# Performance work log

Measured on AMD Instinct MI355X. Metric: run time of the kernel, lower is better.

Reference implementation:

```python
import jax, jax.numpy as jnp
import numpy as np
import math

H = 256  # hidden dim hardcoded in module; d_k = 256
EPS = 1e-5  # torch LayerNorm eps


def _mlp2(x, W1, b1, W2, b2):
    # nn.Sequential(Linear, Tanh, Linear, Tanh)
    return jnp.tanh(jnp.tanh(x @ W1 + b1) @ W2 + b2)


def _ln(x, w, b):
    mu = x.mean(-1, keepdims=True)
    var = ((x - mu) ** 2).mean(-1, keepdims=True)
    return (x - mu) / jnp.sqrt(var + EPS) * w + b


def setup_inputs():
    B, N, D, A = 128, 32, 128, 16
    key = jax.random.key(0)
    ks = jax.random.split(key, 32)

    def lin(k, i, o):
        return jax.random.normal(k, (i, o), jnp.float32) / np.sqrt(i).astype(np.float32)

    inp = {
        'states': jax.random.normal(ks[0], (B, N, D), jnp.float32),
        'policies': jax.nn.softmax(jax.random.normal(ks[1], (B, N, A), jnp.float32), axis=-1),
        'actions': jax.nn.one_hot(jax.random.randint(ks[2], (B, N), 0, A), A, dtype=jnp.float32),
    }
    # two-layer MLP params: state_embed(se), key(k), query(q), state_act_embed(sa),
    # attention_value(av), curr_agent_state_embed(ca)
    ins = {'se': D, 'k': H, 'q': H, 'sa': D + A, 'av': H, 'ca': D}
    i = 3
    for n in ['se', 'k', 'q', 'sa', 'av', 'ca']:
        inp[n + '_W1'] = lin(ks[i], ins[n], H); inp[n + '_b1'] = jnp.zeros((H,), jnp.float32)
        inp[n + '_W2'] = lin(ks[i + 1], H, H);  inp[n + '_b2'] = jnp.zeros((H,), jnp.float32)
        i += 2
    inp['f_W1'] = lin(ks[i], 2 * H, H); inp['f_b1'] = jnp.zeros((H,), jnp.float32); i += 1
    inp['f_W2'] = lin(ks[i], H, H);     inp['f_b2'] = jnp.zeros((H,), jnp.float32); i += 1
    inp['f_W3'] = lin(ks[i], H, A);     inp['f_b3'] = jnp.zeros((A,), jnp.float32); i += 1
    inp['ln1_w'] = jnp.ones((H,), jnp.float32); inp['ln1_b'] = jnp.zeros((H,), jnp.float32)
    inp['ln2_w'] = jnp.ones((H,), jnp.float32); inp['ln2_b'] = jnp.zeros((H,), jnp.float32)
    return inp


def reference(states, policies, actions,
              se_W1, se_b1, se_W2, se_b2,
              k_W1, k_b1, k_W2, k_b2,
              q_W1, q_b1, q_W2, q_b2,
              sa_W1, sa_b1, sa_W2, sa_b2,
              av_W1, av_b1, av_W2, av_b2,
              ca_W1, ca_b1, ca_W2, ca_b2,
              f_W1, f_b1, f_W2, f_b2, f_W3, f_b3,
              ln1_w, ln1_b, ln2_w, ln2_b):
    B, N, D = states.shape
    # remove_self_loops: per-agent gather of all other agents (static index map)
    nbr = np.array([[j for j in range(N) if j != i] for i in range(N)])  # [N, N-1]
    states_key = states[:, nbr, :]        # [B,N,N-1,D]
    actions_nb = actions[:, nbr, :]       # [B,N,N-1,A]
    obs_actions = jnp.concatenate([states_key, actions_nb], axis=-1)

    sq_embed = _mlp2(states, se_W1, se_b1, se_W2, se_b2)       # [B,N,256] (query path)
    sk_embed = _mlp2(states_key, se_W1, se_b1, se_W2, se_b2)   # [B,N,N-1,256]
    key_obs = _mlp2(sk_embed, k_W1, k_b1, k_W2, k_b2)          # [B,N,N-1,256]
    query_obs = _mlp2(sq_embed, q_W1, q_b1, q_W2, q_b2)        # [B,N,256]

    scores = jnp.einsum('bnd,bnmd->bnm', query_obs, key_obs) / math.sqrt(float(H))
    weight = jax.nn.softmax(scores, axis=-1)                   # [B,N,N-1]

    # weight_assignment: insert 1.0 at the self position
    rows = np.arange(N)[:, None]
    weights_full = jnp.zeros((B, N, N), weight.dtype).at[:, rows, nbr].set(weight)
    weights_full = weights_full.at[:, np.arange(N), np.arange(N)].set(1.0)

    oa_embed = _mlp2(obs_actions, sa_W1, sa_b1, sa_W2, sa_b2)  # [B,N,N-1,256]
    att_vals = _mlp2(oa_embed, av_W1, av_b1, av_W2, av_b2)     # [B,N,N-1,256]
    node_feat = jnp.einsum('bnm,bnmd->bnd', weight, att_vals)  # [B,N,256]
    node_feat = _ln(oa_embed.mean(axis=-2) + node_feat, ln1_w, ln1_b)

    cur = _mlp2(states, ca_W1, ca_b1, ca_W2, ca_b2)
    cur = _ln(cur + sk_embed.mean(axis=-2) + sq_embed, ln2_w, ln2_b)

    feat = jnp.concatenate([cur, node_feat], axis=-1)          # [B,N,512]
    h = jnp.tanh(feat @ f_W1 + f_b1)
    h = jnp.tanh(h @ f_W2 + f_b2)
    Q = h @ f_W3 + f_b3                                        # [B,N,A]

    Value = jnp.einsum('bna,bma->bnm', Q, policies)            # Q @ policies^T -> [B,N,N]
    Q_value = jnp.sum(actions * Q, axis=-1, keepdims=True)     # [B,N,1]
    return Value, Q_value, weights_full
```

## Files before the change

kernel.cpp:

```cpp
#include <hip/hip_runtime.h>
#include <hip/hip_bf16.h>


struct Ptrs37 { const void* p[37]; };
struct Meta37 { int sz[37]; unsigned off[37]; };
struct PrepW  { int widx[14]; unsigned dstOff[14]; int K[14]; int Kp[14]; };

typedef __attribute__((ext_vector_type(8))) short bf16x8;
typedef __attribute__((ext_vector_type(4))) float f32x4;

__device__ __forceinline__ bool is_bf16_env(const void* ln1w) {
  return (*(const unsigned int*)ln1w) != 0x3f800000u;
}
__device__ __forceinline__ unsigned short f2bf(float f) {
  union { __hip_bfloat16 h; unsigned short u; } cv;
  cv.h = __float2bfloat16(f);
  return cv.u;
}
__device__ __forceinline__ float bf2f(unsigned short s) {
  return __uint_as_float(((unsigned int)s) << 16);
}
__device__ __forceinline__ float4 ldbf4(const unsigned short* p) {
  uint2 u = *(const uint2*)p;
  const unsigned short* s = (const unsigned short*)&u;
  return make_float4(bf2f(s[0]), bf2f(s[1]), bf2f(s[2]), bf2f(s[3]));
}

__global__ __launch_bounds__(256) void prep_all_kernel(Ptrs37 P, Meta37 M, PrepW pw,
                                                       float* __restrict__ F,
                                                       unsigned short* __restrict__ WT,
                                                       unsigned short* __restrict__ OAin) {
  bool bf = is_bf16_env(P.p[33]);
  int y = blockIdx.y;
  int stride = gridDim.x * 256;
  int g0 = blockIdx.x * 256 + threadIdx.x;
  if (y < 37) {
    int n = M.sz[y];
    float* dst = F + M.off[y];
    if (bf) {
      const unsigned short* s = (const unsigned short*)P.p[y];
      for (int idx = g0; idx < n; idx += stride)
        dst[idx] = __uint_as_float(((unsigned int)s[idx]) << 16);
    } else {
      const float* s = (const float*)P.p[y];
      for (int idx = g0; idx < n; idx += stride) dst[idx] = s[idx];
    }
  } else if (y < 51) {
    int t = y - 37;
    const void* src = P.p[pw.widx[t]];
    unsigned short* dst = WT + pw.dstOff[t];
    int K = pw.K[t], Kp = pw.Kp[t];
    int total = 256 * Kp;
    for (int idx = g0; idx < total; idx += stride) {
      int n = idx / Kp, k = idx - n * Kp;
      unsigned short v = 0;
      if (k < K) {
        size_t si = (size_t)k * 256 + n;
        v = bf ? ((const unsigned short*)src)[si] : f2bf(((const float*)src)[si]);
      }
      dst[idx] = v;
    }
  } else {
    const void* S = P.p[0];
    const void* A = P.p[2];
    for (int gid = g0; gid < 4096 * 160; gid += stride) {
      int r = gid / 160, c = gid - r * 160;
      unsigned short v = 0;
      if (c < 128) {
        size_t si = (size_t)r * 128 + c;
        v = bf ? ((const unsigned short*)S)[si] : f2bf(((const float*)S)[si]);
      } else if (c < 144) {
        size_t si = (size_t)r * 16 + (c - 128);
        v = bf ? ((const unsigned short*)A)[si] : f2bf(((const float*)A)[si]);
      }
      OAin[gid] = v;
    }
  }
}

struct GemmDesc {
  const unsigned short* X; const unsigned short* WT; const float* bias;
  unsigned short* Y; int K; int ldx;
};
struct GemmStage { GemmDesc g[3]; };

__global__ __launch_bounds__(256) void gemm_mfma_kernel(GemmStage st) {
  GemmDesc d = st.g[blockIdx.z];
  const unsigned short* __restrict__ X = d.X;
  const unsigned short* __restrict__ WT = d.WT;
  const int K = d.K;
  __shared__ uint4 AsB[2][256];
  __shared__ uint4 BsB[2][256];
  const int tid = threadIdx.x;
  const int l = tid & 63, w = tid >> 6;
  const int m0 = blockIdx.y << 6, n0 = blockIdx.x << 6;
  const int wm = w >> 1, wn = w & 1;
  const int arow = wm * 32 + (l & 15);
  const int brow = wn * 32 + (l & 15);
  const int koff = (l >> 4) * 8;
  const unsigned short* ag = X + (size_t)(m0 + (tid >> 2)) * d.ldx + (tid & 3) * 8;
  const unsigned short* bg = WT + (size_t)(n0 + (tid >> 2)) * K + (tid & 3) * 8;
  f32x4 acc[2][2] = {};
  AsB[0][tid] = *(const uint4*)ag;
  BsB[0][tid] = *(const uint4*)bg;
  __syncthreads();
  int cur = 0;
  for (int k0 = 0; k0 < K; k0 += 32) {
    const bool more = (k0 + 32) < K;
    uint4 na, nb;
    if (more) {
      na = *(const uint4*)(ag + k0 + 32);
      nb = *(const uint4*)(bg + k0 + 32);
    }
    const char* Ab = (const char*)AsB[cur];
    const char* Bb = (const char*)BsB[cur];
    bf16x8 a0 = *(const bf16x8*)(Ab + arow * 64 + koff * 2);
    bf16x8 a1 = *(const bf16x8*)(Ab + (arow + 16) * 64 + koff * 2);
    bf16x8 b0 = *(const bf16x8*)(Bb + brow * 64 + koff * 2);
    bf16x8 b1 = *(const bf16x8*)(Bb + (brow + 16) * 64 + koff * 2);
    acc[0][0] = __builtin_amdgcn_mfma_f32_16x16x32_bf16(a0, b0, acc[0][0], 0, 0, 0);
    acc[0][1] = __builtin_amdgcn_mfma_f32_16x16x32_bf16(a0, b1, acc[0][1], 0, 0, 0);
    acc[1][0] = __builtin_amdgcn_mfma_f32_16x16x32_bf16(a1, b0, acc[1][0], 0, 0, 0);
    acc[1][1] = __builtin_amdgcn_mfma_f32_16x16x32_bf16(a1, b1, acc[1][1], 0, 0, 0);
    if (more) {
      AsB[cur ^ 1][tid] = na;
      BsB[cur ^ 1][tid] = nb;
      __syncthreads();
      cur ^= 1;
    }
  }
  const float* __restrict__ Bv = d.bias;
  __hip_bfloat16* __restrict__ Y = (__hip_bfloat16*)d.Y;
  const int col0 = n0 + wn * 32 + (l & 15);
  const int rbase = m0 + wm * 32 + (l >> 4) * 4;
#pragma unroll
  for (int ni = 0; ni < 2; ++ni) {
    int col = col0 + ni * 16;
    float bias = Bv[col];
#pragma unroll
    for (int mi = 0; mi < 2; ++mi) {
#pragma unroll
      for (int r = 0; r < 4; ++r) {
        int row = rbase + mi * 16 + r;
        Y[(size_t)row * 256 + col] = __float2bfloat16(tanhf(acc[mi][ni][r] + bias));
      }
    }
  }
}

__global__ __launch_bounds__(256) void attn_kernel(
    const unsigned short* __restrict__ Qb, const unsigned short* __restrict__ Kb,
    const unsigned short* __restrict__ AVp, const unsigned short* __restrict__ OAp,
    const unsigned short* __restrict__ SEp,
    float* __restrict__ NF, float* __restrict__ sumOA, float* __restrict__ sumSE,
    void* __restrict__ dout, const void* __restrict__ ln1w) {
  const size_t WF_OFF = 135168;
  int b = blockIdx.x;
  int tid = threadIdx.x;
  bool bf = is_bf16_env(ln1w);
  __shared__ float AVs[32 * 260];
  __shared__ float wsT[32][36];

  const unsigned short* avg = AVp + (size_t)b * 8192;
  for (int i = tid * 4; i < 8192; i += 1024) {
    int j = i >> 8, c = i & 255;
    *(float4*)&AVs[j * 260 + c] = ldbf4(avg + i);
  }
  {
    int c = tid;
    float sa = 0.f, ss = 0.f;
    const unsigned short* oab = OAp + (size_t)b * 8192 + c;
    const unsigned short* seb = SEp + (size_t)b * 8192 + c;
#pragma unroll 4
    for (int j = 0; j < 32; ++j) { sa += bf2f(oab[j * 256]); ss += bf2f(seb[j * 256]); }
    sumOA[b * 256 + c] = sa;
    sumSE[b * 256 + c] = ss;
  }

  int l = tid & 63, w = tid >> 6;
  int j = l & 31, h = l >> 5;
  const unsigned short* kbase = Kb + (size_t)b * 8192 + j * 256 + h * 128;
  const unsigned short* qbase = Qb + (size_t)b * 8192 + h * 128;
  for (int q = 0; q < 2; ++q) {
    int n0 = w * 8 + q * 4;
    float acc0 = 0.f, acc1 = 0.f, acc2 = 0.f, acc3 = 0.f;
    for (int t = 0; t < 32; ++t) {
      float4 kv = ldbf4(kbase + t * 4);
      float4 q0 = ldbf4(qbase + (n0 + 0) * 256 + t * 4);
      float4 q1 = ldbf4(qbase + (n0 + 1) * 256 + t * 4);
      float4 q2 = ldbf4(qbase + (n0 + 2) * 256 + t * 4);
      float4 q3 = ldbf4(qbase + (n0 + 3) * 256 + t * 4);
      acc0 += q0.x * kv.x + q0.y * kv.y + q0.z * kv.z + q0.w * kv.w;
      acc1 += q1.x * kv.x + q1.y * kv.y + q1.z * kv.z + q1.w * kv.w;
      acc2 += q2.x * kv.x + q2.y * kv.y + q2.z * kv.z + q2.w * kv.w;
      acc3 += q3.x * kv.x + q3.y * kv.y + q3.z * kv.z + q3.w * kv.w;
    }
#pragma unroll
    for (int i = 0; i < 4; ++i) {
      float part = (i == 0) ? acc0 : (i == 1) ? acc1 : (i == 2) ? acc2 : acc3;
      float full = part + __shfl_down(part, 32);
      int n = n0 + i;
      float sc = full * 0.0625f;
      if (j == n) sc = -1e30f;
      float mx = sc;
      mx = fmaxf(mx, __shfl_xor(mx, 16));
      mx = fmaxf(mx, __shfl_xor(mx, 8));
      mx = fmaxf(mx, __shfl_xor(mx, 4));
      mx = fmaxf(mx, __shfl_xor(mx, 2));
      mx = fmaxf(mx, __shfl_xor(mx, 1));
      float e = __expf(sc - mx);
      float s = e;
      s += __shfl_xor(s, 16); s += __shfl_xor(s, 8); s += __shfl_xor(s, 4);
      s += __shfl_xor(s, 2);  s += __shfl_xor(s, 1);
      float wgt = e / s;
      if (l < 32) {
        wsT[j][n] = wgt;
        size_t oi = WF_OFF + ((size_t)(b * 32 + n)) * 32 + j;
        float ov = (j == n) ? 1.0f : wgt;
        if (bf) ((__hip_bfloat16*)dout)[oi] = __float2bfloat16(ov);
        else    ((float*)dout)[oi] = ov;
      }
    }
  }
  __syncthreads();

  int tx = tid & 63, tyy = tid >> 6;
  float accn[8][4] = {};
  for (int jj = 0; jj < 32; ++jj) {
    float4 av = *(const float4*)&AVs[jj * 260 + (tx << 2)];
    const float* wr = &wsT[jj][tyy * 8];
#pragma unroll
    for (int g = 0; g < 8; ++g) {
      float wv = wr[g];
      accn[g][0] += av.x * wv; accn[g][1] += av.y * wv;
      accn[g][2] += av.z * wv; accn[g][3] += av.w * wv;
    }
  }
#pragma unroll
  for (int g = 0; g < 8; ++g) {
    float4 o = make_float4(accn[g][0], accn[g][1], accn[g][2], accn[g][3]);
    *(float4*)&NF[((size_t)(b * 32 + tyy * 8 + g)) * 256 + (tx << 2)] = o;
  }
}

__global__ __launch_bounds__(64) void ln_kernel(
    const float* __restrict__ NF, const float* __restrict__ sOA, const unsigned short* __restrict__ OAp,
    const unsigned short* __restrict__ Cc, const float* __restrict__ sSE, const unsigned short* __restrict__ SEp,
    const float* __restrict__ w1, const float* __restrict__ b1,
    const float* __restrict__ w2, const float* __restrict__ b2,
    unsigned short* __restrict__ feat) {
  int row = blockIdx.x, b = row >> 5, l = threadIdx.x;
  float x[4], y[4];
#pragma unroll
  for (int i = 0; i < 4; ++i) {
    int c = l + (i << 6);
    float oa = bf2f(OAp[row * 256 + c]);
    float se = bf2f(SEp[row * 256 + c]);
    x[i] = NF[row * 256 + c] + (sOA[b * 256 + c] - oa) * (1.0f / 31.0f);
    y[i] = bf2f(Cc[row * 256 + c]) + (sSE[b * 256 + c] - se) * (1.0f / 31.0f) + se;
  }
  float sx = x[0] + x[1] + x[2] + x[3];
  float sy = y[0] + y[1] + y[2] + y[3];
  for (int d = 1; d < 64; d <<= 1) { sx += __shfl_xor(sx, d); sy += __shfl_xor(sy, d); }
  float mx = sx * (1.0f / 256.0f), my = sy * (1.0f / 256.0f);
  float vx = 0.f, vy = 0.f;
#pragma unroll
  for (int i = 0; i < 4; ++i) {
    float dx = x[i] - mx; vx += dx * dx;
    float dy = y[i] - my; vy += dy * dy;
  }
  for (int d = 1; d < 64; d <<= 1) { vx += __shfl_xor(vx, d); vy += __shfl_xor(vy, d); }
  float rx = rsqrtf(vx * (1.0f / 256.0f) + 1e-5f);
  float ry = rsqrtf(vy * (1.0f / 256.0f) + 1e-5f);
#pragma unroll
  for (int i = 0; i < 4; ++i) {
    int c = l + (i << 6);
    feat[(size_t)row * 512 + 256 + c] = f2bf((x[i] - mx) * rx * w1[c] + b1[c]);
    feat[(size_t)row * 512 + c]       = f2bf((y[i] - my) * ry * w2[c] + b2[c]);
  }
}

__global__ __launch_bounds__(256) void qfinal_kernel(const unsigned short* __restrict__ H2,
                                                     const float* __restrict__ W3,
                                                     const float* __restrict__ b3,
                                                     const float* __restrict__ POL,
                                                     const float* __restrict__ ACT,
                                                     void* __restrict__ dout,
                                                     const void* __restrict__ ln1w) {
  bool bf = is_bf16_env(ln1w);
  int b = blockIdx.x, tid = threadIdx.x;
  __shared__ float h2s[32 * 256];
  __shared__ float w3s[256 * 16];
  __shared__ float qfs[512], pols[512], acts[512];
  {
    const unsigned short* src = H2 + (size_t)b * 8192;
#pragma unroll
    for (int i = 0; i < 4; ++i) {
      int base = (tid + i * 256) * 8;
      uint4 u = *(const uint4*)(src + base);
      const unsigned short* s = (const unsigned short*)&u;
#pragma unroll
      for (int e = 0; e < 8; ++e) h2s[base + e] = bf2f(s[e]);
    }
    const float4* wsrc = (const float4*)W3;
    float4* wdst = (float4*)w3s;
#pragma unroll
    for (int i = 0; i < 4; ++i) wdst[tid + i * 256] = wsrc[tid + i * 256];
  }
  for (int i = tid; i < 512; i += 256) {
    pols[i] = POL[(size_t)b * 512 + i];
    acts[i] = ACT[(size_t)b * 512 + i];
  }
  __syncthreads();
#pragma unroll
  for (int t = 0; t < 2; ++t) {
    int p = tid + t * 256;
    int row = p >> 4, a = p & 15;
    float acc = b3[a];
#pragma unroll 8
    for (int k = 0; k < 256; ++k) acc += h2s[row * 256 + k] * w3s[k * 16 + a];
    qfs[p] = acc;
  }
  __syncthreads();
#pragma unroll
  for (int r = 0; r < 4; ++r) {
    int p = tid + (r << 8);
    int n = p >> 5, m = p & 31;
    float acc = 0.f;
#pragma unroll
    for (int a = 0; a < 16; ++a) acc += qfs[n * 16 + a] * pols[m * 16 + a];
    size_t oi = (size_t)b * 1024 + p;
    if (bf) ((__hip_bfloat16*)dout)[oi] = __float2bfloat16(acc);
    else    ((float*)dout)[oi] = acc;
  }
  if (tid < 32) {
    float acc = 0.f;
#pragma unroll
    for (int a = 0; a < 16; ++a) acc += acts[tid * 16 + a] * qfs[tid * 16 + a];
    size_t oi = 131072 + (size_t)b * 32 + tid;
    if (bf) ((__hip_bfloat16*)dout)[oi] = __float2bfloat16(acc);
    else    ((float*)dout)[oi] = acc;
  }
}

extern "C" void kernel_launch(void* const* d_in, const int* in_sizes, int n_in,
                              void* d_out, int out_size, void* d_ws, size_t ws_size,
                              hipStream_t stream) {
  (void)n_in; (void)out_size; (void)ws_size;
  Ptrs37 P; Meta37 M;
  unsigned off = 0;
  for (int i = 0; i < 37; ++i) {
    P.p[i] = d_in[i];
    M.sz[i] = in_sizes[i];
    M.off[i] = off;
    off += (unsigned)in_sizes[i];
  }
  float* F = (float*)d_ws;
  const unsigned MEG = 1048576u;
  unsigned X0 = (off + 511u) & ~511u;
  auto BUF = [&](int slot) { return (unsigned short*)(F + X0 + slot * MEG); };
  unsigned short* SE   = BUF(0);
  unsigned short* QB   = BUF(1);
  unsigned short* KB   = BUF(2);
  unsigned short* OA   = BUF(3);
  unsigned short* AV   = BUF(4);
  unsigned short* CC   = BUF(5);
  unsigned short* T1   = BUF(6);
  unsigned short* T2   = BUF(7);
  unsigned short* T3   = BUF(8);
  float*          NF   = F + X0 + 9 * MEG;
  unsigned short* FEAT = BUF(10);
  unsigned short* OAIN = BUF(12);
  unsigned short* H1   = BUF(13);
  unsigned short* H2   = BUF(14);
  float* SOA  = F + X0 + 15 * MEG;
  float* SSE  = SOA + 32768;
  unsigned short* WT = (unsigned short*)(F + X0 + 16 * MEG);
  auto Wp = [&](int i) { return F + M.off[i]; };
  const void* ln1w_raw = d_in[33];

  static const int wIdx[14] = {3,5,7,9,11,13,15,17,19,21,23,25,27,29};
  PrepW pw{};
  unsigned wtOff[37] = {};
  int Kp_[37] = {};
  unsigned cum = 0;
  for (int t = 0; t < 14; ++t) {
    int i = wIdx[t];
    int K = in_sizes[i] / 256;
    int Kp = (K + 31) & ~31;
    pw.widx[t] = i;
    pw.dstOff[t] = cum;
    pw.K[t] = K; pw.Kp[t] = Kp;
    wtOff[i] = cum; Kp_[i] = Kp;
    cum += (unsigned)(256 * Kp);
  }

  prep_all_kernel<<<dim3(64, 52), 256, 0, stream>>>(P, M, pw, F, WT, OAIN);

  auto G = [&](const unsigned short* X, int ldx, int wi, int bi, unsigned short* Y) {
    GemmDesc g; g.X = X; g.WT = WT + wtOff[wi]; g.bias = Wp(bi); g.Y = Y;
    g.K = Kp_[wi]; g.ldx = ldx;
    return g;
  };
  dim3 gg3(4, 64, 3), gg1(4, 64, 1);
  GemmStage s1{{ G(OAIN, 160, 3, 4, T1),  G(OAIN, 160, 15, 16, T2), G(OAIN, 160, 23, 24, T3) }};
  gemm_mfma_kernel<<<gg3, 256, 0, stream>>>(s1);
  GemmStage s2{{ G(T1, 256, 5, 6, SE),  G(T2, 256, 17, 18, OA),  G(T3, 256, 25, 26, CC) }};
  gemm_mfma_kernel<<<gg3, 256, 0, stream>>>(s2);
  GemmStage s3{{ G(SE, 256, 7, 8, T1),  G(SE, 256, 11, 12, T2),  G(OA, 256, 19, 20, T3) }};
  gemm_mfma_kernel<<<gg3, 256, 0, stream>>>(s3);
  GemmStage s4{{ G(T1, 256, 9, 10, KB), G(T2, 256, 13, 14, QB), G(T3, 256, 21, 22, AV) }};
  gemm_mfma_kernel<<<gg3, 256, 0, stream>>>(s4);

  attn_kernel<<<128, 256, 0, stream>>>(QB, KB, AV, OA, SE, NF, SOA, SSE, d_out, ln1w_raw);
  ln_kernel<<<4096, 64, 0, stream>>>(NF, SOA, OA, CC, SSE, SE,
                                     Wp(33), Wp(34), Wp(35), Wp(36), FEAT);

  GemmDesc g5 = G(FEAT, 512, 27, 28, H1);
  GemmStage s5{{ g5, g5, g5 }};
  gemm_mfma_kernel<<<gg1, 256, 0, stream>>>(s5);
  GemmDesc g6 = G(H1, 256, 29, 30, H2);
  GemmStage s6{{ g6, g6, g6 }};
  gemm_mfma_kernel<<<gg1, 256, 0, stream>>>(s6);

  qfinal_kernel<<<128, 256, 0, stream>>>(H2, Wp(31), Wp(32),
                                         F + M.off[1], F + M.off[2], d_out, ln1w_raw);
}
```

Measured before the change: 237.8 us.

## Fuse two-layer MLP GEMM pairs, attention with LayerNorm, and tail MLP into single kernels

Replaces the per-layer GEMM launches with an mlp2 kernel that computes both linear+tanh layers for a 32-row tile, keeping the intermediate activations in shared memory. Attention and LayerNorm are merged so node features and column sums stay in LDS. The final two GEMMs and the Q/Value computation are merged into one tail kernel. This removes several launches and the global round trips for intermediates. In exchange, grids shrink to 384 or 128 blocks, and each block reloads the full weight matrices.

Result: slower. 287.3 us (+20.8%).

```diff
diff --git a/kernel.cpp b/kernel.cpp
--- a/kernel.cpp
+++ b/kernel.cpp
@@ -78,81 +78,148 @@
   }
 }
 
-struct GemmDesc {
-  const unsigned short* X; const unsigned short* WT; const float* bias;
-  unsigned short* Y; int K; int ldx;
+struct Mlp2Desc {
+  const unsigned short* X; int ldx; int K1;
+  const unsigned short* W1T; const float* b1;
+  const unsigned short* W2T; const float* b2;
+  unsigned short* Y;
 };
-struct GemmStage { GemmDesc g[3]; };
-
-__global__ __launch_bounds__(256) void gemm_mfma_kernel(GemmStage st) {
-  GemmDesc d = st.g[blockIdx.z];
-  const unsigned short* __restrict__ X = d.X;
-  const unsigned short* __restrict__ WT = d.WT;
-  const int K = d.K;
-  __shared__ uint4 AsB[2][256];
-  __shared__ uint4 BsB[2][256];
+struct Mlp2Stage { Mlp2Desc g[3]; };
+
+__global__ __launch_bounds__(256) void mlp2_kernel(Mlp2Stage st) {
+  Mlp2Desc d = st.g[blockIdx.y];
   const int tid = threadIdx.x;
   const int l = tid & 63, w = tid >> 6;
-  const int m0 = blockIdx.y << 6, n0 = blockIdx.x << 6;
-  const int wm = w >> 1, wn = w & 1;
-  const int arow = wm * 32 + (l & 15);
-  const int brow = wn * 32 + (l & 15);
-  const int koff = (l >> 4) * 8;
-  const unsigned short* ag = X + (size_t)(m0 + (tid >> 2)) * d.ldx + (tid & 3) * 8;
-  const unsigned short* bg = WT + (size_t)(n0 + (tid >> 2)) * K + (tid & 3) * 8;
-  f32x4 acc[2][2] = {};
-  AsB[0][tid] = *(const uint4*)ag;
-  BsB[0][tid] = *(const uint4*)bg;
-  __syncthreads();
-  int cur = 0;
-  for (int k0 = 0; k0 < K; k0 += 32) {
-    const bool more = (k0 + 32) < K;
-    uint4 na, nb;
-    if (more) {
-      na = *(const uint4*)(ag + k0 + 32);
-      nb = *(const uint4*)(bg + k0 + 32);
-    }
-    const char* Ab = (const char*)AsB[cur];
-    const char* Bb = (const char*)BsB[cur];
-    bf16x8 a0 = *(const bf16x8*)(Ab + arow * 64 + koff * 2);
-    bf16x8 a1 = *(const bf16x8*)(Ab + (arow + 16) * 64 + koff * 2);
-    bf16x8 b0 = *(const bf16x8*)(Bb + brow * 64 + koff * 2);
-    bf16x8 b1 = *(const bf16x8*)(Bb + (brow + 16) * 64 + koff * 2);
-    acc[0][0] = __builtin_amdgcn_mfma_f32_16x16x32_bf16(a0, b0, acc[0][0], 0, 0, 0);
-    acc[0][1] = __builtin_amdgcn_mfma_f32_16x16x32_bf16(a0, b1, acc[0][1], 0, 0, 0);
-    acc[1][0] = __builtin_amdgcn_mfma_f32_16x16x32_bf16(a1, b0, acc[1][0], 0, 0, 0);
-    acc[1][1] = __builtin_amdgcn_mfma_f32_16x16x32_bf16(a1, b1, acc[1][1], 0, 0, 0);
-    if (more) {
-      AsB[cur ^ 1][tid] = na;
-      BsB[cur ^ 1][tid] = nb;
-      __syncthreads();
-      cur ^= 1;
-    }
-  }
-  const float* __restrict__ Bv = d.bias;
-  __hip_bfloat16* __restrict__ Y = (__hip_bfloat16*)d.Y;
-  const int col0 = n0 + wn * 32 + (l & 15);
-  const int rbase = m0 + wm * 32 + (l >> 4) * 4;
-#pragma unroll
-  for (int ni = 0; ni < 2; ++ni) {
-    int col = col0 + ni * 16;
-    float bias = Bv[col];
-#pragma unroll
-    for (int mi = 0; mi < 2; ++mi) {
-#pragma unroll
-      for (int r = 0; r < 4; ++r) {
-        int row = rbase + mi * 16 + r;
-        Y[(size_t)row * 256 + col] = __float2bfloat16(tanhf(acc[mi][ni][r] + bias));
-      }
-    }
-  }
-}
-
-__global__ __launch_bounds__(256) void attn_kernel(
+  const int lane16 = l & 15, quad = l >> 4;
+  const int m0 = blockIdx.x << 5;
+  __shared__ uint4 A1[2][128];
+  __shared__ uint4 Bt[2][1024];
+  __shared__ unsigned short Y1[32 * 264];
+  const int bcol = tid >> 2, bchk = tid & 3;
+  {
+    const int K1 = d.K1;
+    const unsigned short* ag = d.X + (size_t)(m0 + (tid >> 2)) * d.ldx + (tid & 3) * 8;
+    const unsigned short* w1 = d.W1T;
+    f32x4 acc[2][4] = {};
+    if (tid < 128) A1[0][tid] = *(const uint4*)ag;
+#pragma unroll
+    for (int i = 0; i < 4; ++i) {
+      int c = bcol + (i << 6);
+      Bt[0][c * 4 + bchk] = *(const uint4*)(w1 + (size_t)c * K1 + bchk * 8);
+    }
+    __syncthreads();
+    int cur = 0;
+    for (int k0 = 0; k0 < K1; k0 += 32) {
+      const bool more = (k0 + 32) < K1;
+      uint4 na, nb[4];
+      if (more) {
+        if (tid < 128) na = *(const uint4*)(ag + k0 + 32);
+#pragma unroll
+        for (int i = 0; i < 4; ++i) {
+          int c = bcol + (i << 6);
+          nb[i] = *(const uint4*)(w1 + (size_t)c * K1 + k0 + 32 + bchk * 8);
+        }
+      }
+      const char* Ab = (const char*)A1[cur];
+      const char* Bb = (const char*)Bt[cur];
+      bf16x8 a0 = *(const bf16x8*)(Ab + lane16 * 64 + quad * 16);
+      bf16x8 a1 = *(const bf16x8*)(Ab + (lane16 + 16) * 64 + quad * 16);
+#pragma unroll
+      for (int ni = 0; ni < 4; ++ni) {
+        int cc = (w << 6) + ni * 16 + lane16;
+        bf16x8 b = *(const bf16x8*)(Bb + cc * 64 + quad * 16);
+        acc[0][ni] = __builtin_amdgcn_mfma_f32_16x16x32_bf16(a0, b, acc[0][ni], 0, 0, 0);
+        acc[1][ni] = __builtin_amdgcn_mfma_f32_16x16x32_bf16(a1, b, acc[1][ni], 0, 0, 0);
+      }
+      if (more) {
+        if (tid < 128) A1[cur ^ 1][tid] = na;
+#pragma unroll
+        for (int i = 0; i < 4; ++i) {
+          int c = bcol + (i << 6);
+          Bt[cur ^ 1][c * 4 + bchk] = nb[i];
+        }
+        __syncthreads();
+        cur ^= 1;
+      }
+    }
+#pragma unroll
+    for (int ni = 0; ni < 4; ++ni) {
+      int col = (w << 6) + ni * 16 + lane16;
+      float bias = d.b1[col];
+#pragma unroll
+      for (int mi = 0; mi < 2; ++mi) {
+#pragma unroll
+        for (int r = 0; r < 4; ++r) {
+          int row = mi * 16 + quad * 4 + r;
+          Y1[row * 264 + col] = f2bf(tanhf(acc[mi][ni][r] + bias));
+        }
+      }
+    }
+  }
+  __syncthreads();
+  {
+    const unsigned short* w2 = d.W2T;
+    f32x4 acc[2][4] = {};
+#pragma unroll
+    for (int i = 0; i < 4; ++i) {
+      int c = bcol + (i << 6);
+      Bt[0][c * 4 + bchk] = *(const uint4*)(w2 + (size_t)c * 256 + bchk * 8);
+    }
+    __syncthreads();
+    int cur = 0;
+    for (int k0 = 0; k0 < 256; k0 += 32) {
+      const bool more = (k0 + 32) < 256;
+      uint4 nb[4];
+      if (more) {
+#pragma unroll
+        for (int i = 0; i < 4; ++i) {
+          int c = bcol + (i << 6);
+          nb[i] = *(const uint4*)(w2 + (size_t)c * 256 + k0 + 32 + bchk * 8);
+        }
+      }
+      const char* Bb = (const char*)Bt[cur];
+      bf16x8 a0 = *(const bf16x8*)(Y1 + lane16 * 264 + k0 + quad * 8);
+      bf16x8 a1 = *(const bf16x8*)(Y1 + (lane16 + 16) * 264 + k0 + quad * 8);
+#pragma unroll
+      for (int ni = 0; ni < 4; ++ni) {
+        int cc = (w << 6) + ni * 16 + lane16;
+        bf16x8 b = *(const bf16x8*)(Bb + cc * 64 + quad * 16);
+        acc[0][ni] = __builtin_amdgcn_mfma_f32_16x16x32_bf16(a0, b, acc[0][ni], 0, 0, 0);
+        acc[1][ni] = __builtin_amdgcn_mfma_f32_16x16x32_bf16(a1, b, acc[1][ni], 0, 0, 0);
+      }
+      if (more) {
+#pragma unroll
+        for (int i = 0; i < 4; ++i) {
+          int c = bcol + (i << 6);
+          Bt[cur ^ 1][c * 4 + bchk] = nb[i];
+        }
+        __syncthreads();
+        cur ^= 1;
+      }
+    }
+#pragma unroll
+    for (int ni = 0; ni < 4; ++ni) {
+      int col = (w << 6) + ni * 16 + lane16;
+      float bias = d.b2[col];
+#pragma unroll
+      for (int mi = 0; mi < 2; ++mi) {
+#pragma unroll
+        for (int r = 0; r < 4; ++r) {
+          int row = m0 + mi * 16 + quad * 4 + r;
+          d.Y[(size_t)row * 256 + col] = f2bf(tanhf(acc[mi][ni][r] + bias));
+        }
+      }
+    }
+  }
+}
+
+__global__ __launch_bounds__(256) void attnln_kernel(
     const unsigned short* __restrict__ Qb, const unsigned short* __restrict__ Kb,
     const unsigned short* __restrict__ AVp, const unsigned short* __restrict__ OAp,
-    const unsigned short* __restrict__ SEp,
-    float* __restrict__ NF, float* __restrict__ sumOA, float* __restrict__ sumSE,
+    const unsigned short* __restrict__ SEp, const unsigned short* __restrict__ Cc,
+    const float* __restrict__ w1, const float* __restrict__ b1,
+    const float* __restrict__ w2, const float* __restrict__ b2,
+    unsigned short* __restrict__ feat,
     void* __restrict__ dout, const void* __restrict__ ln1w) {
   const size_t WF_OFF = 135168;
   int b = blockIdx.x;
@@ -160,6 +227,7 @@
   bool bf = is_bf16_env(ln1w);
   __shared__ float AVs[32 * 260];
   __shared__ float wsT[32][36];
+  __shared__ float sOAs[256], sSEs[256];
 
   const unsigned short* avg = AVp + (size_t)b * 8192;
   for (int i = tid * 4; i < 8192; i += 1024) {
@@ -173,8 +241,8 @@
     const unsigned short* seb = SEp + (size_t)b * 8192 + c;
 #pragma unroll 4
     for (int j = 0; j < 32; ++j) { sa += bf2f(oab[j * 256]); ss += bf2f(seb[j * 256]); }
-    sumOA[b * 256 + c] = sa;
-    sumSE[b * 256 + c] = ss;
+    sOAs[c] = sa;
+    sSEs[c] = ss;
   }
 
   int l = tid & 63, w = tid >> 6;
@@ -236,80 +304,180 @@
       accn[g][2] += av.z * wv; accn[g][3] += av.w * wv;
     }
   }
+  __syncthreads();
 #pragma unroll
   for (int g = 0; g < 8; ++g) {
     float4 o = make_float4(accn[g][0], accn[g][1], accn[g][2], accn[g][3]);
-    *(float4*)&NF[((size_t)(b * 32 + tyy * 8 + g)) * 256 + (tx << 2)] = o;
-  }
-}
-
-__global__ __launch_bounds__(64) void ln_kernel(
-    const float* __restrict__ NF, const float* __restrict__ sOA, const unsigned short* __restrict__ OAp,
-    const unsigned short* __restrict__ Cc, const float* __restrict__ sSE, const unsigned short* __restrict__ SEp,
-    const float* __restrict__ w1, const float* __restrict__ b1,
-    const float* __restrict__ w2, const float* __restrict__ b2,
-    unsigned short* __restrict__ feat) {
-  int row = blockIdx.x, b = row >> 5, l = threadIdx.x;
-  float x[4], y[4];
-#pragma unroll
-  for (int i = 0; i < 4; ++i) {
-    int c = l + (i << 6);
-    float oa = bf2f(OAp[row * 256 + c]);
-    float se = bf2f(SEp[row * 256 + c]);
-    x[i] = NF[row * 256 + c] + (sOA[b * 256 + c] - oa) * (1.0f / 31.0f);
-    y[i] = bf2f(Cc[row * 256 + c]) + (sSE[b * 256 + c] - se) * (1.0f / 31.0f) + se;
-  }
-  float sx = x[0] + x[1] + x[2] + x[3];
-  float sy = y[0] + y[1] + y[2] + y[3];
-  for (int d = 1; d < 64; d <<= 1) { sx += __shfl_xor(sx, d); sy += __shfl_xor(sy, d); }
-  float mx = sx * (1.0f / 256.0f), my = sy * (1.0f / 256.0f);
-  float vx = 0.f, vy = 0.f;
-#pragma unroll
-  for (int i = 0; i < 4; ++i) {
-    float dx = x[i] - mx; vx += dx * dx;
-    float dy = y[i] - my; vy += dy * dy;
-  }
-  for (int d = 1; d < 64; d <<= 1) { vx += __shfl_xor(vx, d); vy += __shfl_xor(vy, d); }
-  float rx = rsqrtf(vx * (1.0f / 256.0f) + 1e-5f);
-  float ry = rsqrtf(vy * (1.0f / 256.0f) + 1e-5f);
-#pragma unroll
-  for (int i = 0; i < 4; ++i) {
-    int c = l + (i << 6);
-    feat[(size_t)row * 512 + 256 + c] = f2bf((x[i] - mx) * rx * w1[c] + b1[c]);
-    feat[(size_t)row * 512 + c]       = f2bf((y[i] - my) * ry * w2[c] + b2[c]);
-  }
-}
-
-__global__ __launch_bounds__(256) void qfinal_kernel(const unsigned short* __restrict__ H2,
-                                                     const float* __restrict__ W3,
-                                                     const float* __restrict__ b3,
-                                                     const float* __restrict__ POL,
-                                                     const float* __restrict__ ACT,
-                                                     void* __restrict__ dout,
-                                                     const void* __restrict__ ln1w) {
+    *(float4*)&AVs[(tyy * 8 + g) * 260 + (tx << 2)] = o;
+  }
+  __syncthreads();
+
+  for (int r = w; r < 32; r += 4) {
+    int row = b * 32 + r;
+    float x[4], y[4];
+#pragma unroll
+    for (int i = 0; i < 4; ++i) {
+      int c = l + (i << 6);
+      float oa = bf2f(OAp[(size_t)row * 256 + c]);
+      float se = bf2f(SEp[(size_t)row * 256 + c]);
+      x[i] = AVs[r * 260 + c] + (sOAs[c] - oa) * (1.0f / 31.0f);
+      y[i] = bf2f(Cc[(size_t)row * 256 + c]) + (sSEs[c] - se) * (1.0f / 31.0f) + se;
+    }
+    float sx = x[0] + x[1] + x[2] + x[3];
+    float sy = y[0] + y[1] + y[2] + y[3];
+    for (int dd = 1; dd < 64; dd <<= 1) { sx += __shfl_xor(sx, dd); sy += __shfl_xor(sy, dd); }
+    float mx = sx * (1.0f / 256.0f), my = sy * (1.0f / 256.0f);
+    float vx = 0.f, vy = 0.f;
+#pragma unroll
+    for (int i = 0; i < 4; ++i) {
+      float dx = x[i] - mx; vx += dx * dx;
+      float dy = y[i] - my; vy += dy * dy;
+    }
+    for (int dd = 1; dd < 64; dd <<= 1) { vx += __shfl_xor(vx, dd); vy += __shfl_xor(vy, dd); }
+    float rx = rsqrtf(vx * (1.0f / 256.0f) + 1e-5f);
+    float ry = rsqrtf(vy * (1.0f / 256.0f) + 1e-5f);
+#pragma unroll
+    for (int i = 0; i < 4; ++i) {
+      int c = l + (i << 6);
+      feat[(size_t)row * 512 + 256 + c] = f2bf((x[i] - mx) * rx * w1[c] + b1[c]);
+      feat[(size_t)row * 512 + c]       = f2bf((y[i] - my) * ry * w2[c] + b2[c]);
+    }
+  }
+}
+
+__global__ __launch_bounds__(256) void tail_kernel(
+    const unsigned short* __restrict__ FEAT,
+    const unsigned short* __restrict__ W1T,
+    const float* __restrict__ fb1,
+    const unsigned short* __restrict__ W2T,
+    const float* __restrict__ fb2,
+    const float* __restrict__ W3,
+    const float* __restrict__ b3,
+    const float* __restrict__ POL, const float* __restrict__ ACT,
+    void* __restrict__ dout, const void* __restrict__ ln1w) {
   bool bf = is_bf16_env(ln1w);
   int b = blockIdx.x, tid = threadIdx.x;
-  __shared__ float h2s[32 * 256];
-  __shared__ float w3s[256 * 16];
-  __shared__ float qfs[512], pols[512], acts[512];
-  {
-    const unsigned short* src = H2 + (size_t)b * 8192;
-#pragma unroll
-    for (int i = 0; i < 4; ++i) {
-      int base = (tid + i * 256) * 8;
-      uint4 u = *(const uint4*)(src + base);
-      const unsigned short* s = (const unsigned short*)&u;
-#pragma unroll
-      for (int e = 0; e < 8; ++e) h2s[base + e] = bf2f(s[e]);
-    }
-    const float4* wsrc = (const float4*)W3;
-    float4* wdst = (float4*)w3s;
-#pragma unroll
-    for (int i = 0; i < 4; ++i) wdst[tid + i * 256] = wsrc[tid + i * 256];
-  }
+  const int l = tid & 63, w = tid >> 6;
+  const int lane16 = l & 15, quad = l >> 4;
+  __shared__ uint4 Bt[1024];
+  __shared__ unsigned short H1[32 * 264];
+  __shared__ unsigned short H2[32 * 256];
+  __shared__ float qfs[512];
+  __shared__ float pols[512], acts[512];
+  const int bcol = tid >> 2, bchk = tid & 3;
   for (int i = tid; i < 512; i += 256) {
     pols[i] = POL[(size_t)b * 512 + i];
     acts[i] = ACT[(size_t)b * 512 + i];
+  }
+  {
+    const unsigned short* ax0 = FEAT + (size_t)(b * 32 + lane16) * 512 + quad * 8;
+    const unsigned short* ax1 = ax0 + (size_t)16 * 512;
+    f32x4 acc[2][4] = {};
+    uint4 a0c = *(const uint4*)ax0;
+    uint4 a1c = *(const uint4*)ax1;
+#pragma unroll
+    for (int i = 0; i < 4; ++i) {
+      int c = bcol + (i << 6);
+      Bt[c * 4 + bchk] = *(const uint4*)(W1T + (size_t)c * 512 + bchk * 8);
+    }
+    __syncthreads();
+    for (int k0 = 0; k0 < 512; k0 += 32) {
+      const bool more = (k0 + 32) < 512;
+      uint4 na0, na1, nb[4];
+      if (more) {
+        na0 = *(const uint4*)(ax0 + k0 + 32);
+        na1 = *(const uint4*)(ax1 + k0 + 32);
+#pragma unroll
+        for (int i = 0; i < 4; ++i) {
+          int c = bcol + (i << 6);
+          nb[i] = *(const uint4*)(W1T + (size_t)c * 512 + k0 + 32 + bchk * 8);
+        }
+      }
+      bf16x8 a0 = *(const bf16x8*)&a0c;
+      bf16x8 a1 = *(const bf16x8*)&a1c;
+#pragma unroll
+      for (int ni = 0; ni < 4; ++ni) {
+        int cc = (w << 6) + ni * 16 + lane16;
+        bf16x8 bb = *(const bf16x8*)((const char*)Bt + cc * 64 + quad * 16);
+        acc[0][ni] = __builtin_amdgcn_mfma_f32_16x16x32_bf16(a0, bb, acc[0][ni], 0, 0, 0);
+        acc[1][ni] = __builtin_amdgcn_mfma_f32_16x16x32_bf16(a1, bb, acc[1][ni], 0, 0, 0);
+      }
+      if (more) {
+        __syncthreads();
+#pragma unroll
+        for (int i = 0; i < 4; ++i) {
+          int c = bcol + (i << 6);
+          Bt[c * 4 + bchk] = nb[i];
+        }
+        a0c = na0; a1c = na1;
+        __syncthreads();
+      }
+    }
+#pragma unroll
+    for (int ni = 0; ni < 4; ++ni) {
+      int col = (w << 6) + ni * 16 + lane16;
+      float bias = fb1[col];
+#pragma unroll
+      for (int mi = 0; mi < 2; ++mi) {
+#pragma unroll
+        for (int r = 0; r < 4; ++r) {
+          int row = mi * 16 + quad * 4 + r;
+          H1[row * 264 + col] = f2bf(tanhf(acc[mi][ni][r] + bias));
+        }
+      }
+    }
+  }
+  __syncthreads();
+  {
+    f32x4 acc[2][4] = {};
+#pragma unroll
+    for (int i = 0; i < 4; ++i) {
+      int c = bcol + (i << 6);
+      Bt[c * 4 + bchk] = *(const uint4*)(W2T + (size_t)c * 256 + bchk * 8);
+    }
+    __syncthreads();
+    for (int k0 = 0; k0 < 256; k0 += 32) {
+      const bool more = (k0 + 32) < 256;
+      uint4 nb[4];
+      if (more) {
+#pragma unroll
+        for (int i = 0; i < 4; ++i) {
+          int c = bcol + (i << 6);
+          nb[i] = *(const uint4*)(W2T + (size_t)c * 256 + k0 + 32 + bchk * 8);
+        }
+      }
+      bf16x8 a0 = *(const bf16x8*)(H1 + lane16 * 264 + k0 + quad * 8);
+      bf16x8 a1 = *(const bf16x8*)(H1 + (lane16 + 16) * 264 + k0 + quad * 8);
+#pragma unroll
+      for (int ni = 0; ni < 4; ++ni) {
+        int cc = (w << 6) + ni * 16 + lane16;
+        bf16x8 bb = *(const bf16x8*)((const char*)Bt + cc * 64 + quad * 16);
+        acc[0][ni] = __builtin_amdgcn_mfma_f32_16x16x32_bf16(a0, bb, acc[0][ni], 0, 0, 0);
+        acc[1][ni] = __builtin_amdgcn_mfma_f32_16x16x32_bf16(a1, bb, acc[1][ni], 0, 0, 0);
+      }
+      if (more) {
+        __syncthreads();
+#pragma unroll
+        for (int i = 0; i < 4; ++i) {
+          int c = bcol + (i << 6);
+          Bt[c * 4 + bchk] = nb[i];
+        }
+        __syncthreads();
+      }
+    }
+#pragma unroll
+    for (int ni = 0; ni < 4; ++ni) {
+      int col = (w << 6) + ni * 16 + lane16;
+      float bias = fb2[col];
+#pragma unroll
+      for (int mi = 0; mi < 2; ++mi) {
+#pragma unroll
+        for (int r = 0; r < 4; ++r) {
+          int row = mi * 16 + quad * 4 + r;
+          H2[row * 256 + col] = f2bf(tanhf(acc[mi][ni][r] + bias));
+        }
+      }
+    }
   }
   __syncthreads();
 #pragma unroll
@@ -318,7 +486,7 @@
     int row = p >> 4, a = p & 15;
     float acc = b3[a];
 #pragma unroll 8
-    for (int k = 0; k < 256; ++k) acc += h2s[row * 256 + k] * w3s[k * 16 + a];
+    for (int k = 0; k < 256; ++k) acc += bf2f(H2[row * 256 + k]) * W3[k * 16 + a];
     qfs[p] = acc;
   }
   __syncthreads();
@@ -365,17 +533,9 @@
   unsigned short* OA   = BUF(3);
   unsigned short* AV   = BUF(4);
   unsigned short* CC   = BUF(5);
-  unsigned short* T1   = BUF(6);
-  unsigned short* T2   = BUF(7);
-  unsigned short* T3   = BUF(8);
-  float*          NF   = F + X0 + 9 * MEG;
-  unsigned short* FEAT = BUF(10);
-  unsigned short* OAIN = BUF(12);
-  unsigned short* H1   = BUF(13);
-  unsigned short* H2   = BUF(14);
-  float* SOA  = F + X0 + 15 * MEG;
-  float* SSE  = SOA + 32768;
-  unsigned short* WT = (unsigned short*)(F + X0 + 16 * MEG);
+  unsigned short* FEAT = BUF(6);
+  unsigned short* OAIN = BUF(8);
+  unsigned short* WT = (unsigned short*)(F + X0 + 9 * MEG);
   auto Wp = [&](int i) { return F + M.off[i]; };
   const void* ln1w_raw = d_in[33];
 
@@ -397,32 +557,31 @@
 
   prep_all_kernel<<<dim3(64, 52), 256, 0, stream>>>(P, M, pw, F, WT, OAIN);
 
-  auto G = [&](const unsigned short* X, int ldx, int wi, int bi, unsigned short* Y) {
-    GemmDesc g; g.X = X; g.WT = WT + wtOff[wi]; g.bias = Wp(bi); g.Y = Y;
-    g.K = Kp_[wi]; g.ldx = ldx;
+  auto M2 = [&](const unsigned short* X, int ldx, int w1i, int b1i, int w2i, int b2i,
+                unsigned short* Y) {
+    Mlp2Desc g;
+    g.X = X; g.ldx = ldx; g.K1 = Kp_[w1i];
+    g.W1T = WT + wtOff[w1i]; g.b1 = Wp(b1i);
+    g.W2T = WT + wtOff[w2i]; g.b2 = Wp(b2i);
+    g.Y = Y;
     return g;
   };
-  dim3 gg3(4, 64, 3), gg1(4, 64, 1);
-  GemmStage s1{{ G(OAIN, 160, 3, 4, T1),  G(OAIN, 160, 15, 16, T2), G(OAIN, 160, 23, 24, T3) }};
-  gemm_mfma_kernel<<<gg3, 256, 0, stream>>>(s1);
-  GemmStage s2{{ G(T1, 256, 5, 6, SE),  G(T2, 256, 17, 18, OA),  G(T3, 256, 25, 26, CC) }};
-  gemm_mfma_kernel<<<gg3, 256, 0, stream>>>(s2);
-  GemmStage s3{{ G(SE, 256, 7, 8, T1),  G(SE, 256, 11, 12, T2),  G(OA, 256, 19, 20, T3) }};
-  gemm_mfma_kernel<<<gg3, 256, 0, stream>>>(s3);
-  GemmStage s4{{ G(T1, 256, 9, 10, KB), G(T2, 256, 13, 14, QB), G(T3, 256, 21, 22, AV) }};
-  gemm_mfma_kernel<<<gg3, 256, 0, stream>>>(s4);
-
-  attn_kernel<<<128, 256, 0, stream>>>(QB, KB, AV, OA, SE, NF, SOA, SSE, d_out, ln1w_raw);
-  ln_kernel<<<4096, 64, 0, stream>>>(NF, SOA, OA, CC, SSE, SE,
-                                     Wp(33), Wp(34), Wp(35), Wp(36), FEAT);
-
-  GemmDesc g5 = G(FEAT, 512, 27, 28, H1);
-  GemmStage s5{{ g5, g5, g5 }};
-  gemm_mfma_kernel<<<gg1, 256, 0, stream>>>(s5);
-  GemmDesc g6 = G(H1, 256, 29, 30, H2);
-  GemmStage s6{{ g6, g6, g6 }};
-  gemm_mfma_kernel<<<gg1, 256, 0, stream>>>(s6);
-
-  qfinal_kernel<<<128, 256, 0, stream>>>(H2, Wp(31), Wp(32),
-                                         F + M.off[1], F + M.off[2], d_out, ln1w_raw);
-}
+  Mlp2Stage sA{{ M2(OAIN, 160, 3, 4, 5, 6, SE),
+                 M2(OAIN, 160, 15, 16, 17, 18, OA),
+                 M2(OAIN, 160, 23, 24, 25, 26, CC) }};
+  mlp2_kernel<<<dim3(128, 3), 256, 0, stream>>>(sA);
+  Mlp2Stage sB{{ M2(SE, 256, 7, 8, 9, 10, KB),
+                 M2(SE, 256, 11, 12, 13, 14, QB),
+                 M2(OA, 256, 19, 20, 21, 22, AV) }};
+  mlp2_kernel<<<dim3(128, 3), 256, 0, stream>>>(sB);
+
+  attnln_kernel<<<128, 256, 0, stream>>>(QB, KB, AV, OA, SE, CC,
+                                         Wp(33), Wp(34), Wp(35), Wp(36),
+                                         FEAT, d_out, ln1w_raw);
+
+  tail_kernel<<<128, 256, 0, stream>>>(FEAT, WT + wtOff[27], Wp(28),
+                                       WT + wtOff[29], Wp(30),
+                                       Wp(31), Wp(32),
+                                       F + M.off[1], F + M.off[2],
+                                       d_out, ln1w_raw);
+}
```
